# Kernel optimization log

Hardware: AMD Instinct MI355X
Metric: run time of the kernel (lower is better)

The kernel has to match this reference:

```python
import jax, jax.numpy as jnp
import numpy as np

D = 256      # d_model
K = 8        # knn neighbors
Q = 2048     # num queries
N = 32768    # num superpoints
H = 8        # mamba heads (d_inner/head_dim)
HD = 64      # head_dim
ST = 64      # state_size
DIN = H * HD                 # 512, expand*d_model
CONV = DIN + 2 * ST          # 640
NPROJ = 2 * DIN + 2 * ST + H # 1160
HID = 1024   # ffn hidden
NL = 2       # ssm layers
KC = 4       # conv kernel


def _ln(x, eps=1e-5):
    m = x.mean(-1, keepdims=True)
    v = ((x - m) ** 2).mean(-1, keepdims=True)
    return (x - m) * jax.lax.rsqrt(v + eps)


def _silu(x):
    return x * jax.nn.sigmoid(x)


def _mamba2(x, Win, Wconv, bconv, A_log, Dh, dtb, rmsw, Wout):
    # x: [B, L, D]; faithful HF Mamba2Mixer recurrent form
    B, L, _ = x.shape
    proj = x @ Win.T  # [B,L,NPROJ]
    z, xBC, dt = jnp.split(proj, [DIN, DIN + CONV], axis=-1)
    # causal depthwise conv1d, kernel KC, left pad KC-1
    xp = jnp.pad(xBC, ((0, 0), (KC - 1, 0), (0, 0)))
    conv = sum(xp[:, j:j + L, :] * Wconv[:, j] for j in range(KC))
    xBC = _silu(conv + bconv)
    xs, Bm, Cm = jnp.split(xBC, [DIN, DIN + ST], axis=-1)
    dt = jax.nn.softplus(dt + dtb)  # [B,L,H]
    A = -jnp.exp(A_log)             # [H]
    xh = xs.reshape(B, L, H, HD)
    dA = jnp.exp(dt * A)            # [B,L,H]
    dBx = dt[..., None, None] * Bm[:, :, None, None, :] * xh[..., None]  # [B,L,H,HD,ST]

    def step(h, inp):
        dA_t, dBx_t, C_t = inp
        h = h * dA_t[..., None, None] + dBx_t
        y = jnp.einsum('bhds,bs->bhd', h, C_t)
        return h, y

    h0 = jnp.zeros((B, H, HD, ST), x.dtype)
    _, ys = jax.lax.scan(step, h0, (dA.transpose(1, 0, 2),
                                    dBx.transpose(1, 0, 2, 3, 4),
                                    Cm.transpose(1, 0, 2)))
    y = ys.transpose(1, 0, 2, 3) + Dh[None, None, :, None] * xh
    y = y.reshape(B, L, DIN) * _silu(z)  # gated RMSNorm
    y = y * jax.lax.rsqrt((y * y).mean(-1, keepdims=True) + 1e-5) * rmsw
    return y @ Wout.T


def setup_inputs() -> dict:
    key = jax.random.key(0)
    ks = jax.random.split(key, 32)
    s = 0.02
    rn = lambda i, sh: jax.random.normal(ks[i], sh, jnp.float32) * s
    inp = {
        'query': jax.random.normal(ks[0], (Q, D), jnp.float32),
        'query_pos': jax.random.uniform(ks[1], (Q, 3), jnp.float32),
        'inst_feats': jax.random.normal(ks[2], (N, D), jnp.float32),
        'sp_coords': jax.random.uniform(ks[3], (N, 3), jnp.float32),
        'w_q': rn(4, (D, D)), 'w_v': rn(5, (D, D)), 'w_o': rn(6, (D, D)),
        'w_k': rn(7, (K, D)), 'w_b': jnp.zeros((K,), jnp.float32),
        'ssm_Win': rn(8, (NL, NPROJ, D)),
        'ssm_Wconv': rn(9, (NL, CONV, KC)),
        'ssm_bconv': jnp.zeros((NL, CONV), jnp.float32),
        'ssm_Alog': jnp.log(jnp.broadcast_to(jnp.arange(1, H + 1, dtype=jnp.float32), (NL, H))),
        'ssm_D': jnp.ones((NL, H), jnp.float32),
        'ssm_dtb': jax.random.uniform(ks[10], (NL, H), jnp.float32) * 0.1,
        'ssm_rmsw': jnp.ones((NL, DIN), jnp.float32),
        'ssm_Wout': rn(11, (NL, D, DIN)),
        'ffn_w1': rn(12, (HID, D)), 'ffn_b1': jnp.zeros((HID,), jnp.float32),
        'ffn_w2': rn(13, (D, HID)), 'ffn_b2': jnp.zeros((D,), jnp.float32),
        'order': jnp.stack([jax.random.permutation(ks[14], Q),
                            jax.random.permutation(ks[15], Q)]).astype(jnp.int32),
    }
    return inp


def reference(query, query_pos, inst_feats, sp_coords,
              w_q, w_v, w_o, w_k, w_b,
              ssm_Win, ssm_Wconv, ssm_bconv, ssm_Alog, ssm_D, ssm_dtb, ssm_rmsw, ssm_Wout,
              ffn_w1, ffn_b1, ffn_w2, ffn_b2, order):
    # --- MambaAggregation: KNN group + small-K softmax mixing ---
    d2 = (query_pos ** 2).sum(-1, keepdims=True) + (sp_coords ** 2).sum(-1)[None, :] \
         - 2.0 * query_pos @ sp_coords.T  # [Q,N]
    _, idx = jax.lax.top_k(-d2, K)        # [Q,K] nearest neighbors
    feat = inst_feats[idx]                # [Q,K,D]
    q = query @ w_q.T
    v = feat @ w_v.T
    kw = jax.nn.softmax(q @ w_k.T + w_b, axis=-1)          # [Q,K]
    w = jnp.einsum('qk,qd,qkd->qd', kw, q, v)
    x = _ln(w @ w_o.T + query)

    # --- SSM: serialize along 2 orders, Mamba2 mix, unsort, average ---
    inv = jnp.argsort(order, axis=1)  # [2,Q]
    for l in range(NL):
        sc = x
        xn = _ln(x)
        xs = xn[order]  # [2,Q,D], two serialization paths as batch
        y = _mamba2(xs, ssm_Win[l], ssm_Wconv[l], ssm_bconv[l], ssm_Alog[l],
                    ssm_D[l], ssm_dtb[l], ssm_rmsw[l], ssm_Wout[l])
        back = jnp.take_along_axis(y, inv[:, :, None], axis=1)  # undo sort
        x = _ln(sc + back.mean(0))

    # --- FFN ---
    h = jax.nn.gelu(x @ ffn_w1.T + ffn_b1, approximate=False) @ ffn_w2.T + ffn_b2
    return _ln(x + h)
```

## Files before the change

### kernel.cpp

```cpp
#include <hip/hip_runtime.h>
#include <cstdint>


typedef __attribute__((ext_vector_type(8))) short bf16x8;
typedef __attribute__((ext_vector_type(4))) float f32x4;
typedef unsigned short ushort_t;

__device__ __forceinline__ unsigned short f2bf(float f) {
  unsigned int u = __float_as_uint(f);
  u += 0x7fff + ((u >> 16) & 1);
  return (unsigned short)(u >> 16);
}
__device__ __forceinline__ float bf2f(unsigned short h) {
  return __uint_as_float(((unsigned int)h) << 16);
}

__global__ __launch_bounds__(256) void cvt_kernel(
    const float* __restrict__ src, unsigned short* __restrict__ hi,
    unsigned short* __restrict__ lo, int n4)
{
  const int i = blockIdx.x*256 + threadIdx.x;
  if (i < n4) {
    const float4 v = ((const float4*)src)[i];
    const unsigned short h0=f2bf(v.x), h1=f2bf(v.y), h2=f2bf(v.z), h3=f2bf(v.w);
    const unsigned short l0=f2bf(v.x-bf2f(h0)), l1=f2bf(v.y-bf2f(h1)),
                         l2=f2bf(v.z-bf2f(h2)), l3=f2bf(v.w-bf2f(h3));
    ((uint2*)hi)[i] = make_uint2((unsigned)h0 | ((unsigned)h1<<16),
                                 (unsigned)h2 | ((unsigned)h3<<16));
    ((uint2*)lo)[i] = make_uint2((unsigned)l0 | ((unsigned)l1<<16),
                                 (unsigned)l2 | ((unsigned)l3<<16));
  }
}

#define KNN_INS_U(ukv, uiv)                                                    \
  do {                                                                         \
    const unsigned int _k = (ukv); const int _v = (uiv);                       \
    const bool a0 = _k < k0;                                                   \
    const bool a1 = _k < k1;                                                   \
    const bool a2 = _k < k2;                                                   \
    const bool a3 = _k < k3;                                                   \
    const bool a4 = _k < k4;                                                   \
    const bool a5 = _k < k5;                                                   \
    const bool a6 = _k < k6;                                                   \
    k7 = a6 ? k6 : _k;              id7 = a6 ? id6 : _v;                       \
    k6 = a5 ? k5 : (a6 ? _k : k6);  id6 = a5 ? id5 : (a6 ? _v : id6);          \
    k5 = a4 ? k4 : (a5 ? _k : k5);  id5 = a4 ? id4 : (a5 ? _v : id5);          \
    k4 = a3 ? k3 : (a4 ? _k : k4);  id4 = a3 ? id3 : (a4 ? _v : id4);          \
    k3 = a2 ? k2 : (a3 ? _k : k3);  id3 = a2 ? id2 : (a3 ? _v : id3);          \
    k2 = a1 ? k1 : (a2 ? _k : k2);  id2 = a1 ? id1 : (a2 ? _v : id2);          \
    k1 = a0 ? k0 : (a1 ? _k : k1);  id1 = a0 ? id0 : (a1 ? _v : id1);          \
    k0 = a0 ? _k : k0;              id0 = a0 ? _v : id0;                       \
  } while (0)

__device__ __forceinline__ bool ulex_less(unsigned int k, int i,
                                          unsigned int kr, int ir) {
  return k < kr || (k == kr && i < ir);
}

#define KNN_INS_ULEX(ukv, uiv)                                                 \
  do {                                                                         \
    const unsigned int _k = (ukv); const int _v = (uiv);                       \
    const bool a0 = ulex_less(_k, _v, k0, id0);                                \
    const bool a1 = ulex_less(_k, _v, k1, id1);                                \
    const bool a2 = ulex_less(_k, _v, k2, id2);                                \
    const bool a3 = ulex_less(_k, _v, k3, id3);                                \
    const bool a4 = ulex_less(_k, _v, k4, id4);                                \
    const bool a5 = ulex_less(_k, _v, k5, id5);                                \
    const bool a6 = ulex_less(_k, _v, k6, id6);                                \
    k7 = a6 ? k6 : _k;              id7 = a6 ? id6 : _v;                       \
    k6 = a5 ? k5 : (a6 ? _k : k6);  id6 = a5 ? id5 : (a6 ? _v : id6);          \
    k5 = a4 ? k4 : (a5 ? _k : k5);  id5 = a4 ? id4 : (a5 ? _v : id5);          \
    k4 = a3 ? k3 : (a4 ? _k : k4);  id4 = a3 ? id3 : (a4 ? _v : id4);          \
    k3 = a2 ? k2 : (a3 ? _k : k3);  id3 = a2 ? id2 : (a3 ? _v : id3);          \
    k2 = a1 ? k1 : (a2 ? _k : k2);  id2 = a1 ? id1 : (a2 ? _v : id2);          \
    k1 = a0 ? k0 : (a1 ? _k : k1);  id1 = a0 ? id0 : (a1 ? _v : id1);          \
    k0 = a0 ? _k : k0;              id0 = a0 ? _v : id0;                       \
  } while (0)

#define KNN_RESET_U()                                                          \
  do {                                                                         \
    k0=k1=k2=k3=k4=k5=k6=k7 = 0xFFFFFFFFu;                                     \
    id0=id1=id2=id3=id4=id5=id6=id7 = 0x7fffffff;                              \
  } while (0)

__global__ void prep_kernel(const float* __restrict__ spos,
                            float4* __restrict__ P4)
{
#pragma clang fp contract(off)
  const int n = blockIdx.x*256 + threadIdx.x;
  if (n < 32768) {
    const float sx = spos[n*3+0], sy = spos[n*3+1], sz = spos[n*3+2];
    P4[n] = make_float4(sx, sy, sz, sx*sx + sy*sy + sz*sz);
  }
}

__global__ __launch_bounds__(256) void knn_kernel(
    const float* __restrict__ qpos, const float4* __restrict__ P4,
    int* __restrict__ idx_out)
{
#pragma clang fp contract(off)
  __shared__ unsigned int skey[32];
  __shared__ int          sidx[32];
  const int q = blockIdx.x, tid = threadIdx.x;
  const int wave = tid >> 6, lane = tid & 63;
  const float qx = qpos[q*3+0], qy = qpos[q*3+1], qz = qpos[q*3+2];
  const float qq = qx*qx + qy*qy + qz*qz;
  unsigned int k0,k1,k2,k3,k4,k5,k6,k7;
  int          id0,id1,id2,id3,id4,id5,id6,id7;
  KNN_RESET_U();
  const int base = wave << 13;
  for (int it = 0; it < 128; ++it) {
    const int nb = base + (it << 6);
    const float4 p = P4[nb + lane];
    const float dot = qx*p.x + qy*p.y + qz*p.z;
    const float d2 = (qq + p.w) - 2.0f*dot;
    unsigned int u = __float_as_uint(d2);
    u ^= (unsigned int)((int)u >> 31) | 0x80000000u;
    unsigned long long m = __ballot(u < k7);
    if (m) {
      do {
        const int l = __ffsll(m) - 1;
        m &= m - 1;
        const unsigned int uk = (unsigned int)__shfl((int)u, l);
        if (uk < k7) {
          KNN_INS_U(uk, nb + l);
        }
      } while (m);
    }
  }
  if (lane == 0) {
    skey[wave*8+0]=k0; skey[wave*8+1]=k1; skey[wave*8+2]=k2; skey[wave*8+3]=k3;
    skey[wave*8+4]=k4; skey[wave*8+5]=k5; skey[wave*8+6]=k6; skey[wave*8+7]=k7;
    sidx[wave*8+0]=id0; sidx[wave*8+1]=id1; sidx[wave*8+2]=id2; sidx[wave*8+3]=id3;
    sidx[wave*8+4]=id4; sidx[wave*8+5]=id5; sidx[wave*8+6]=id6; sidx[wave*8+7]=id7;
  }
  __syncthreads();
  if (tid == 0) {
    KNN_RESET_U();
    for (int s = 0; s < 32; ++s) {
      const unsigned int uk = skey[s];
      const int          ui = sidx[s];
      if (ulex_less(uk, ui, k7, id7)) KNN_INS_ULEX(uk, ui);
    }
    idx_out[q*8+0]=id0; idx_out[q*8+1]=id1; idx_out[q*8+2]=id2; idx_out[q*8+3]=id3;
    idx_out[q*8+4]=id4; idx_out[q*8+5]=id5; idx_out[q*8+6]=id6; idx_out[q*8+7]=id7;
  }
}

__global__ void inv_kernel(const int* __restrict__ order, int* __restrict__ inv)
{
  int i = blockIdx.x*blockDim.x + threadIdx.x;
  if (i < 4096) { int b = i >> 11, t = i & 2047; inv[(b<<11) + order[i]] = t; }
}

#define GBM 128
#define GBN 64
#define GBK 32
#define GLDK 40
__global__ __launch_bounds__(256) void gemm_mfma(
    const unsigned short* __restrict__ Ahp, const unsigned short* __restrict__ Alp,
    const int* __restrict__ rowmap,
    const unsigned short* __restrict__ Bhp, const unsigned short* __restrict__ Blp,
    const float* __restrict__ bias,
    float* __restrict__ Y, int M, int Nn, int Kd, int act)
{
  __shared__ unsigned short Ah[GBM*GLDK], Al[GBM*GLDK];
  __shared__ unsigned short Bh[GBN*GLDK], Bl[GBN*GLDK];
  const int tid = threadIdx.x;
  const int bm = blockIdx.x, bn = blockIdx.y;
  const int wid = tid >> 6, lane = tid & 63;
  const int wr = wid >> 1, wc = wid & 1;
  const int l15 = lane & 15, lk = (lane >> 4) << 3;

  const int sar = tid >> 1, sak = (tid & 1) << 4;
  const int agrow = bm*GBM + sar;
  const int asrc = rowmap ? rowmap[agrow] : agrow;
  const unsigned short* ArH = Ahp + (size_t)asrc * Kd + sak;
  const unsigned short* ArL = Alp + (size_t)asrc * Kd + sak;
  const int sbr = tid >> 2, sbk = (tid & 3) << 3;
  const int wrow = bn*GBN + sbr;
  const bool bok = (wrow < Nn);
  const unsigned short* BrH = Bhp + (size_t)(bok ? wrow : 0) * Kd + sbk;
  const unsigned short* BrL = Blp + (size_t)(bok ? wrow : 0) * Kd + sbk;

  f32x4 acc[4][2];
#pragma unroll
  for (int m = 0; m < 4; ++m)
#pragma unroll
    for (int n = 0; n < 2; ++n) acc[m][n] = (f32x4){0.f,0.f,0.f,0.f};

  const uint4 z4 = make_uint4(0u,0u,0u,0u);
  for (int k0 = 0; k0 < Kd; k0 += GBK) {
    const int ao = sar*GLDK + sak;
    *(uint4*)&Ah[ao]     = *(const uint4*)(ArH + k0);
    *(uint4*)&Ah[ao + 8] = *(const uint4*)(ArH + k0 + 8);
    *(uint4*)&Al[ao]     = *(const uint4*)(ArL + k0);
    *(uint4*)&Al[ao + 8] = *(const uint4*)(ArL + k0 + 8);
    const int bo = sbr*GLDK + sbk;
    *(uint4*)&Bh[bo] = bok ? *(const uint4*)(BrH + k0) : z4;
    *(uint4*)&Bl[bo] = bok ? *(const uint4*)(BrL + k0) : z4;
    __syncthreads();
    bf16x8 afh[4], afl[4], bfh[2], bfl[2];
#pragma unroll
    for (int m = 0; m < 4; ++m) {
      const int row = wr*64 + m*16 + l15;
      afh[m] = *(const bf16x8*)&Ah[row*GLDK + lk];
      afl[m] = *(const bf16x8*)&Al[row*GLDK + lk];
    }
#pragma unroll
    for (int n = 0; n < 2; ++n) {
      const int row = wc*32 + n*16 + l15;
      bfh[n] = *(const bf16x8*)&Bh[row*GLDK + lk];
      bfl[n] = *(const bf16x8*)&Bl[row*GLDK + lk];
    }
#pragma unroll
    for (int m = 0; m < 4; ++m)
#pragma unroll
      for (int n = 0; n < 2; ++n) {
        acc[m][n] = __builtin_amdgcn_mfma_f32_16x16x32_bf16(afh[m], bfh[n], acc[m][n], 0,0,0);
        acc[m][n] = __builtin_amdgcn_mfma_f32_16x16x32_bf16(afh[m], bfl[n], acc[m][n], 0,0,0);
        acc[m][n] = __builtin_amdgcn_mfma_f32_16x16x32_bf16(afl[m], bfh[n], acc[m][n], 0,0,0);
      }
    __syncthreads();
  }
  const int crow0 = bm*GBM + wr*64 + (lane >> 4)*4;
#pragma unroll
  for (int m = 0; m < 4; ++m) {
#pragma unroll
    for (int n = 0; n < 2; ++n) {
      const int col = bn*GBN + wc*32 + n*16 + l15;
      if (col < Nn) {
#pragma unroll
        for (int r = 0; r < 4; ++r) {
          float v = acc[m][n][r];
          if (bias) v += bias[col];
          if (act == 1) v = 0.5f*v*(1.f + erff(v*0.7071067811865475f));
          Y[(size_t)(crow0 + m*16 + r)*Nn + col] = v;
        }
      }
    }
  }
}

__global__ __launch_bounds__(256) void kwmix_kernel(
    const float* __restrict__ QP, const float* __restrict__ wk,
    const float* __restrict__ wb, const float* __restrict__ V,
    float* __restrict__ W)
{
  const int wave = threadIdx.x >> 6, lane = threadIdx.x & 63;
  const int q = blockIdx.x*4 + wave;
  float qv[4];
#pragma unroll
  for (int j = 0; j < 4; ++j) qv[j] = QP[(size_t)q*256 + lane + 64*j];
  float logit[8];
#pragma unroll
  for (int k = 0; k < 8; ++k) {
    float p = 0.f;
#pragma unroll
    for (int j = 0; j < 4; ++j) p += qv[j]*wk[k*256 + lane + 64*j];
    for (int off = 32; off; off >>= 1) p += __shfl_xor(p, off);
    logit[k] = p + wb[k];
  }
  float mx = logit[0];
#pragma unroll
  for (int k = 1; k < 8; ++k) mx = fmaxf(mx, logit[k]);
  float e[8]; float s = 0.f;
#pragma unroll
  for (int k = 0; k < 8; ++k) { e[k] = expf(logit[k]-mx); s += e[k]; }
  float inv = 1.f/s;
  float acc[4] = {0.f,0.f,0.f,0.f};
#pragma unroll
  for (int k = 0; k < 8; ++k) {
    float kwv = e[k]*inv;
#pragma unroll
    for (int j = 0; j < 4; ++j)
      acc[j] = fmaf(kwv, V[(size_t)(q*8+k)*256 + lane + 64*j], acc[j]);
  }
#pragma unroll
  for (int j = 0; j < 4; ++j)
    W[(size_t)q*256 + lane + 64*j] = qv[j]*acc[j];
}

__global__ __launch_bounds__(256) void ln_kernel(
    const float* __restrict__ a, const float* __restrict__ b,
    float* __restrict__ out, int rows)
{
  const int wave = threadIdx.x >> 6, lane = threadIdx.x & 63;
  const int row = blockIdx.x*4 + wave;
  if (row >= rows) return;
  float v[4];
#pragma unroll
  for (int j = 0; j < 4; ++j) {
    float x = a[(size_t)row*256 + lane + 64*j];
    if (b) x += b[(size_t)row*256 + lane + 64*j];
    v[j] = x;
  }
  float s = v[0]+v[1]+v[2]+v[3];
  for (int off = 32; off; off >>= 1) s += __shfl_xor(s, off);
  float m = s * (1.0f/256.0f);
  float t = 0.f;
#pragma unroll
  for (int j = 0; j < 4; ++j) { float d = v[j]-m; t += d*d; }
  for (int off = 32; off; off >>= 1) t += __shfl_xor(t, off);
  float r = rsqrtf(t * (1.0f/256.0f) + 1e-5f);
#pragma unroll
  for (int j = 0; j < 4; ++j)
    out[(size_t)row*256 + lane + 64*j] = (v[j]-m)*r;
}

__global__ __launch_bounds__(256) void ln_unsort_kernel(
    const float* __restrict__ OUTL, const int* __restrict__ INV,
    float* __restrict__ X)
{
  const int wave = threadIdx.x >> 6, lane = threadIdx.x & 63;
  const int q = blockIdx.x*4 + wave;
  const int i0 = INV[q], i1 = INV[2048 + q];
  float v[4];
#pragma unroll
  for (int j = 0; j < 4; ++j) {
    int d = lane + 64*j;
    v[j] = X[(size_t)q*256 + d]
         + 0.5f*(OUTL[(size_t)i0*256 + d] + OUTL[(size_t)(2048+i1)*256 + d]);
  }
  float s = v[0]+v[1]+v[2]+v[3];
  for (int off = 32; off; off >>= 1) s += __shfl_xor(s, off);
  float m = s * (1.0f/256.0f);
  float t = 0.f;
#pragma unroll
  for (int j = 0; j < 4; ++j) { float d = v[j]-m; t += d*d; }
  for (int off = 32; off; off >>= 1) t += __shfl_xor(t, off);
  float r = rsqrtf(t * (1.0f/256.0f) + 1e-5f);
#pragma unroll
  for (int j = 0; j < 4; ++j)
    X[(size_t)q*256 + lane + 64*j] = (v[j]-m)*r;
}

__global__ void conv_kernel(const float* __restrict__ PROJ,
    const float* __restrict__ Wc, const float* __restrict__ bc,
    float* __restrict__ XBC)
{
  const int c = threadIdx.x;
  const int bt = blockIdx.x;
  const int t = bt & 2047;
  float acc = bc[c];
#pragma unroll
  for (int j = 0; j < 4; ++j) {
    int d = j - 3;
    if (t + d >= 0)
      acc = fmaf(PROJ[(size_t)(bt + d)*1160 + 512 + c], Wc[c*4+j], acc);
  }
  XBC[(size_t)bt*640 + c] = acc / (1.f + expf(-acc));
}

__global__ void dta_kernel(const float* __restrict__ PROJ,
    const float* __restrict__ dtb, const float* __restrict__ Alog,
    float* __restrict__ Ddt, float* __restrict__ Dda)
{
  const int i = blockIdx.x*256 + threadIdx.x;
  const int bt = i >> 3, hh = i & 7;
  float x = PROJ[(size_t)bt*1160 + 1152 + hh] + dtb[hh];
  float dt = (x > 20.f) ? x : log1pf(expf(x));
  float A = -expf(Alog[hh]);
  Ddt[hh*4096 + bt] = dt;
  Dda[hh*4096 + bt] = expf(dt * A);
}

__global__ __launch_bounds__(64) void scan1_kernel(
    const float* __restrict__ XBC, const float* __restrict__ Ddt,
    const float* __restrict__ Dda, float* __restrict__ SCH, float* __restrict__ PC)
{
  const int blk = blockIdx.x;
  const int c = blk & 31, hh = (blk >> 5) & 7, b = blk >> 8;
  const int lane = threadIdx.x;
  const int t0 = (b << 11) + (c << 6);
  __shared__ float Bsh[64][64];
  __shared__ float Xsh[64][64];
  __shared__ float dAs[64], dts[64];
#pragma unroll
  for (int it = 0; it < 16; ++it) {
    int idx = it*64 + lane;
    int t = idx >> 4, c4 = (idx & 15) << 2;
    *(float4*)&Bsh[t][c4] = *(const float4*)&XBC[(size_t)(t0 + t)*640 + 512 + c4];
    *(float4*)&Xsh[t][c4] = *(const float4*)&XBC[(size_t)(t0 + t)*640 + (hh<<6) + c4];
  }
  dAs[lane] = Dda[hh*4096 + t0 + lane];
  dts[lane] = Ddt[hh*4096 + t0 + lane];
  __syncthreads();
  float h[64];
#pragma unroll
  for (int s = 0; s < 64; ++s) h[s] = 0.f;
  float p = 1.f;
  for (int t = 0; t < 64; ++t) {
    const float dA = dAs[t];
    const float u = dts[t]*Xsh[t][lane];
    p *= dA;
    const float4* B4 = (const float4*)&Bsh[t][0];
#pragma unroll
    for (int s4 = 0; s4 < 16; ++s4) {
      float4 bv = B4[s4];
      h[4*s4+0] = fmaf(h[4*s4+0], dA, bv.x*u);
      h[4*s4+1] = fmaf(h[4*s4+1], dA, bv.y*u);
      h[4*s4+2] = fmaf(h[4*s4+2], dA, bv.z*u);
      h[4*s4+3] = fmaf(h[4*s4+3], dA, bv.w*u);
    }
  }
  float* op = SCH + (size_t)blk*4096 + lane*64;
#pragma unroll
  for (int s4 = 0; s4 < 16; ++s4)
    ((float4*)op)[s4] = make_float4(h[4*s4], h[4*s4+1], h[4*s4+2], h[4*s4+3]);
  if (lane == 0) PC[blk] = p;
}

__global__ void combine_kernel(float* __restrict__ SCH, const float* __restrict__ PC)
{
  const int tid = blockIdx.x*256 + threadIdx.x;
  const int bh = tid >> 12, ds = tid & 4095;
  float h = 0.f;
  for (int cc = 0; cc < 32; ++cc) {
    size_t o = ((size_t)(bh*32 + cc) << 12) + ds;
    float s = SCH[o];
    SCH[o] = h;
    h = fmaf(h, PC[bh*32+cc], s);
  }
}

__global__ __launch_bounds__(64) void scan2_kernel(
    const float* __restrict__ XBC, const float* __restrict__ Ddt,
    const float* __restrict__ Dda, const float* __restrict__ HST,
    const float* __restrict__ Dm, float* __restrict__ Yout)
{
  const int blk = blockIdx.x;
  const int c = blk & 31, hh = (blk >> 5) & 7, b = blk >> 8;
  const int lane = threadIdx.x;
  const int t0 = (b << 11) + (c << 6);
  __shared__ float Bsh[64][64];
  __shared__ float Csh[64][64];
  __shared__ float Xsh[64][64];
  __shared__ float dAs[64], dts[64];
#pragma unroll
  for (int it = 0; it < 16; ++it) {
    int idx = it*64 + lane;
    int t = idx >> 4, c4 = (idx & 15) << 2;
    *(float4*)&Bsh[t][c4] = *(const float4*)&XBC[(size_t)(t0 + t)*640 + 512 + c4];
    *(float4*)&Csh[t][c4] = *(const float4*)&XBC[(size_t)(t0 + t)*640 + 576 + c4];
    *(float4*)&Xsh[t][c4] = *(const float4*)&XBC[(size_t)(t0 + t)*640 + (hh<<6) + c4];
  }
  dAs[lane] = Dda[hh*4096 + t0 + lane];
  dts[lane] = Ddt[hh*4096 + t0 + lane];
  const float Dh = Dm[hh];
  float h[64];
  const float4* hp = (const float4*)(HST + (size_t)blk*4096 + lane*64);
#pragma unroll
  for (int s4 = 0; s4 < 16; ++s4) {
    float4 t4 = hp[s4];
    h[4*s4+0]=t4.x; h[4*s4+1]=t4.y; h[4*s4+2]=t4.z; h[4*s4+3]=t4.w;
  }
  __syncthreads();
  for (int t = 0; t < 64; ++t) {
    const float dA = dAs[t];
    const float u = dts[t]*Xsh[t][lane];
    float y = 0.f;
    const float4* B4 = (const float4*)&Bsh[t][0];
    const float4* C4 = (const float4*)&Csh[t][0];
#pragma unroll
    for (int s4 = 0; s4 < 16; ++s4) {
      float4 bv = B4[s4];
      float4 cv = C4[s4];
      h[4*s4+0] = fmaf(h[4*s4+0], dA, bv.x*u); y = fmaf(cv.x, h[4*s4+0], y);
      h[4*s4+1] = fmaf(h[4*s4+1], dA, bv.y*u); y = fmaf(cv.y, h[4*s4+1], y);
      h[4*s4+2] = fmaf(h[4*s4+2], dA, bv.z*u); y = fmaf(cv.z, h[4*s4+2], y);
      h[4*s4+3] = fmaf(h[4*s4+3], dA, bv.w*u); y = fmaf(cv.w, h[4*s4+3], y);
    }
    Yout[(size_t)(t0 + t)*512 + (hh<<6) + lane] = y + Dh*Xsh[t][lane];
  }
}

__global__ __launch_bounds__(256) void gaterms_kernel(
    float* __restrict__ Y, const float* __restrict__ PROJ,
    const float* __restrict__ rmsw)
{
  const int wave = threadIdx.x >> 6, lane = threadIdx.x & 63;
  const int row = blockIdx.x*4 + wave;
  float v[8]; float ss = 0.f;
#pragma unroll
  for (int j = 0; j < 8; ++j) {
    float y = Y[(size_t)row*512 + lane + 64*j];
    float z = PROJ[(size_t)row*1160 + lane + 64*j];
    float g = y * (z / (1.f + expf(-z)));
    v[j] = g; ss += g*g;
  }
  for (int off = 32; off; off >>= 1) ss += __shfl_xor(ss, off);
  float r = rsqrtf(ss * (1.0f/512.0f) + 1e-5f);
#pragma unroll
  for (int j = 0; j < 8; ++j)
    Y[(size_t)row*512 + lane + 64*j] = v[j] * r * rmsw[lane + 64*j];
}

extern "C" void kernel_launch(void* const* d_in, const int* in_sizes, int n_in,
                              void* d_out, int out_size, void* d_ws, size_t ws_size,
                              hipStream_t stream)
{
  (void)in_sizes; (void)n_in; (void)out_size; (void)ws_size;
  const float* query = (const float*)d_in[0];
  const float* qpos  = (const float*)d_in[1];
  const float* feats = (const float*)d_in[2];
  const float* spos  = (const float*)d_in[3];
  const float* w_q   = (const float*)d_in[4];
  const float* w_v   = (const float*)d_in[5];
  const float* w_o   = (const float*)d_in[6];
  const float* w_k   = (const float*)d_in[7];
  const float* w_b   = (const float*)d_in[8];
  const float* Win   = (const float*)d_in[9];
  const float* Wconv = (const float*)d_in[10];
  const float* bconv = (const float*)d_in[11];
  const float* Alog  = (const float*)d_in[12];
  const float* Dm    = (const float*)d_in[13];
  const float* dtb   = (const float*)d_in[14];
  const float* rmsw  = (const float*)d_in[15];
  const float* Wout  = (const float*)d_in[16];
  const float* fw1   = (const float*)d_in[17];
  const float* fb1   = (const float*)d_in[18];
  const float* fw2   = (const float*)d_in[19];
  const float* fb2   = (const float*)d_in[20];
  const int*   order = (const int*)d_in[21];
  float* out = (float*)d_out;

  char* ws = (char*)d_ws;
  size_t off = 0;
  auto alloc = [&](size_t bytes) -> void* {
    void* p = ws + off;
    off = (off + bytes + 255) & ~(size_t)255;
    return p;
  };
  int*   IDX = (int*)alloc((size_t)2048*8*4);
  int*   INV = (int*)alloc((size_t)4096*4);
  float* PC  = (float*)alloc((size_t)512*4);
  float4* P4 = (float4*)alloc((size_t)32768*16);
  float* Ddt = (float*)alloc((size_t)4096*8*4);
  float* Dda = (float*)alloc((size_t)4096*8*4);
  float* QP  = (float*)alloc((size_t)2048*256*4);
  float* WB  = (float*)alloc((size_t)2048*256*4);
  float* WO  = (float*)alloc((size_t)2048*256*4);
  float* X   = (float*)alloc((size_t)2048*256*4);
  float* XN  = (float*)alloc((size_t)2048*256*4);
  float* U1  = (float*)alloc((size_t)4096*1160*4);
  float* U2  = (float*)alloc((size_t)4096*640*4);
  float* SCH = (float*)alloc((size_t)512*4096*4);
  float* Yb  = (float*)alloc((size_t)4096*512*4);
  float* U6  = (float*)alloc((size_t)4096*256*4);
  unsigned short* Qh  = (unsigned short*)alloc((size_t)2048*256*2);
  unsigned short* Ql  = (unsigned short*)alloc((size_t)2048*256*2);
  unsigned short* U7h = (unsigned short*)alloc((size_t)32768*256*2);
  unsigned short* U7l = (unsigned short*)alloc((size_t)32768*256*2);
  unsigned short* WBh = (unsigned short*)alloc((size_t)2048*256*2);
  unsigned short* WBl = (unsigned short*)alloc((size_t)2048*256*2);
  unsigned short* XNh = (unsigned short*)alloc((size_t)2048*256*2);
  unsigned short* XNl = (unsigned short*)alloc((size_t)2048*256*2);
  unsigned short* Ybh = (unsigned short*)alloc((size_t)4096*512*2);
  unsigned short* Ybl = (unsigned short*)alloc((size_t)4096*512*2);
  unsigned short* Xh  = (unsigned short*)alloc((size_t)2048*256*2);
  unsigned short* Xl  = (unsigned short*)alloc((size_t)2048*256*2);
  unsigned short* Wqh = (unsigned short*)alloc((size_t)256*256*2);
  unsigned short* Wql = (unsigned short*)alloc((size_t)256*256*2);
  unsigned short* Wvh = (unsigned short*)alloc((size_t)256*256*2);
  unsigned short* Wvl = (unsigned short*)alloc((size_t)256*256*2);
  unsigned short* Woh = (unsigned short*)alloc((size_t)256*256*2);
  unsigned short* Wol = (unsigned short*)alloc((size_t)256*256*2);
  unsigned short* Wih = (unsigned short*)alloc((size_t)2*1160*256*2);
  unsigned short* Wil = (unsigned short*)alloc((size_t)2*1160*256*2);
  unsigned short* Wuh = (unsigned short*)alloc((size_t)2*256*512*2);
  unsigned short* Wul = (unsigned short*)alloc((size_t)2*256*512*2);
  unsigned short* F1h = (unsigned short*)alloc((size_t)1024*256*2);
  unsigned short* F1l = (unsigned short*)alloc((size_t)1024*256*2);
  unsigned short* F2h = (unsigned short*)alloc((size_t)256*1024*2);
  unsigned short* F2l = (unsigned short*)alloc((size_t)256*1024*2);
  float* Vb   = U1;  float* PROJ = U1;
  float* XBC  = U2;  float* FFH  = U2;
  float* OUTL = U6;  float* FFO  = U6;
  unsigned short* FFHh = U7h;
  unsigned short* FFHl = U7l;

  auto cvt = [&](const float* s, unsigned short* h, unsigned short* l, int n) {
    cvt_kernel<<<(n/4 + 255)/256, 256, 0, stream>>>(s, h, l, n/4);
  };

  inv_kernel<<<16, 256, 0, stream>>>(order, INV);
  prep_kernel<<<128, 256, 0, stream>>>(spos, P4);
  knn_kernel<<<2048, 256, 0, stream>>>(qpos, P4, IDX);
  cvt(query, Qh, Ql, 2048*256);
  cvt(feats, U7h, U7l, 32768*256);
  cvt(w_q, Wqh, Wql, 256*256);
  cvt(w_v, Wvh, Wvl, 256*256);
  cvt(w_o, Woh, Wol, 256*256);
  cvt(Win, Wih, Wil, 2*1160*256);
  cvt(Wout, Wuh, Wul, 2*256*512);
  cvt(fw1, F1h, F1l, 1024*256);
  cvt(fw2, F2h, F2l, 256*1024);
  gemm_mfma<<<dim3(16,4), 256, 0, stream>>>(Qh, Ql, nullptr, Wqh, Wql, nullptr,
                                            QP, 2048,256,256,0);
  gemm_mfma<<<dim3(128,4), 256, 0, stream>>>(U7h, U7l, IDX, Wvh, Wvl, nullptr,
                                             Vb, 16384,256,256,0);
  kwmix_kernel<<<512, 256, 0, stream>>>(QP, w_k, w_b, Vb, WB);
  cvt(WB, WBh, WBl, 2048*256);
  gemm_mfma<<<dim3(16,4), 256, 0, stream>>>(WBh, WBl, nullptr, Woh, Wol, nullptr,
                                            WO, 2048,256,256,0);
  ln_kernel<<<512, 256, 0, stream>>>(WO, query, X, 2048);

  for (int l = 0; l < 2; ++l) {
    ln_kernel<<<512, 256, 0, stream>>>(X, nullptr, XN, 2048);
    cvt(XN, XNh, XNl, 2048*256);
    gemm_mfma<<<dim3(32,19), 256, 0, stream>>>(XNh, XNl, order,
                                               Wih + (size_t)l*1160*256,
                                               Wil + (size_t)l*1160*256,
                                               nullptr, PROJ, 4096,1160,256,0);
    conv_kernel<<<4096, 640, 0, stream>>>(PROJ, Wconv + l*640*4, bconv + l*640, XBC);
    dta_kernel<<<128, 256, 0, stream>>>(PROJ, dtb + l*8, Alog + l*8, Ddt, Dda);
    scan1_kernel<<<512, 64, 0, stream>>>(XBC, Ddt, Dda, SCH, PC);
    combine_kernel<<<256, 256, 0, stream>>>(SCH, PC);
    scan2_kernel<<<512, 64, 0, stream>>>(XBC, Ddt, Dda, SCH, Dm + l*8, Yb);
    gaterms_kernel<<<1024, 256, 0, stream>>>(Yb, PROJ, rmsw + l*512);
    cvt(Yb, Ybh, Ybl, 4096*512);
    gemm_mfma<<<dim3(32,4), 256, 0, stream>>>(Ybh, Ybl, nullptr,
                                              Wuh + (size_t)l*256*512,
                                              Wul + (size_t)l*256*512,
                                              nullptr, OUTL, 4096,256,512,0);
    ln_unsort_kernel<<<512, 256, 0, stream>>>(OUTL, INV, X);
  }

  cvt(X, Xh, Xl, 2048*256);
  gemm_mfma<<<dim3(16,16), 256, 0, stream>>>(Xh, Xl, nullptr, F1h, F1l, fb1,
                                             FFH, 2048,1024,256,1);
  cvt(FFH, FFHh, FFHl, 2048*1024);
  gemm_mfma<<<dim3(16,4), 256, 0, stream>>>(FFHh, FFHl, nullptr, F2h, F2l, fb2,
                                            FFO, 2048,256,1024,0);
  ln_kernel<<<512, 256, 0, stream>>>(FFO, X, out, 2048);
}
```

Measured before the change: 601.0 us.

## Fuse bf16 hi/lo splits into producer kernels and batch 4 queries per KNN block

Producer kernels (kwmix, ln, ln_unsort, gaterms, the FFN1 GEMM epilogue) now write the split bf16 hi/lo pair directly. This removes five separate cvt launches plus the fp32 intermediate round-trips. The KNN kernel now handles four queries per block with a prefetched P4 load, so each superpoint load is reused four times. The cost is higher register pressure from four top-8 lists and more divergent insertion loops per wave.

Result: no change. 607.4 us (+1.1%).

```diff
diff --git a/kernel.cpp b/kernel.cpp
--- a/kernel.cpp
+++ b/kernel.cpp
@@ -4,7 +4,6 @@
 
 typedef __attribute__((ext_vector_type(8))) short bf16x8;
 typedef __attribute__((ext_vector_type(4))) float f32x4;
-typedef unsigned short ushort_t;
 
 __device__ __forceinline__ unsigned short f2bf(float f) {
   unsigned int u = __float_as_uint(f);
@@ -32,24 +31,32 @@
   }
 }
 
-#define KNN_INS_U(ukv, uiv)                                                    \
+#define KNN_DECL(i)                                                            \
+  unsigned int k0_##i=0xFFFFFFFFu,k1_##i=0xFFFFFFFFu,k2_##i=0xFFFFFFFFu,       \
+               k3_##i=0xFFFFFFFFu,k4_##i=0xFFFFFFFFu,k5_##i=0xFFFFFFFFu,       \
+               k6_##i=0xFFFFFFFFu,k7_##i=0xFFFFFFFFu;                          \
+  int id0_##i=0x7fffffff,id1_##i=0x7fffffff,id2_##i=0x7fffffff,                \
+      id3_##i=0x7fffffff,id4_##i=0x7fffffff,id5_##i=0x7fffffff,                \
+      id6_##i=0x7fffffff,id7_##i=0x7fffffff
+
+#define KNN_INS_Q(i, ukv, uiv)                                                 \
   do {                                                                         \
     const unsigned int _k = (ukv); const int _v = (uiv);                       \
-    const bool a0 = _k < k0;                                                   \
-    const bool a1 = _k < k1;                                                   \
-    const bool a2 = _k < k2;                                                   \
-    const bool a3 = _k < k3;                                                   \
-    const bool a4 = _k < k4;                                                   \
-    const bool a5 = _k < k5;                                                   \
-    const bool a6 = _k < k6;                                                   \
-    k7 = a6 ? k6 : _k;              id7 = a6 ? id6 : _v;                       \
-    k6 = a5 ? k5 : (a6 ? _k : k6);  id6 = a5 ? id5 : (a6 ? _v : id6);          \
-    k5 = a4 ? k4 : (a5 ? _k : k5);  id5 = a4 ? id4 : (a5 ? _v : id5);          \
-    k4 = a3 ? k3 : (a4 ? _k : k4);  id4 = a3 ? id3 : (a4 ? _v : id4);          \
-    k3 = a2 ? k2 : (a3 ? _k : k3);  id3 = a2 ? id2 : (a3 ? _v : id3);          \
-    k2 = a1 ? k1 : (a2 ? _k : k2);  id2 = a1 ? id1 : (a2 ? _v : id2);          \
-    k1 = a0 ? k0 : (a1 ? _k : k1);  id1 = a0 ? id0 : (a1 ? _v : id1);          \
-    k0 = a0 ? _k : k0;              id0 = a0 ? _v : id0;                       \
+    const bool a0 = _k < k0_##i;                                               \
+    const bool a1 = _k < k1_##i;                                               \
+    const bool a2 = _k < k2_##i;                                               \
+    const bool a3 = _k < k3_##i;                                               \
+    const bool a4 = _k < k4_##i;                                               \
+    const bool a5 = _k < k5_##i;                                               \
+    const bool a6 = _k < k6_##i;                                               \
+    k7_##i = a6 ? k6_##i : _k;                  id7_##i = a6 ? id6_##i : _v;   \
+    k6_##i = a5 ? k5_##i : (a6 ? _k : k6_##i);  id6_##i = a5 ? id5_##i : (a6 ? _v : id6_##i); \
+    k5_##i = a4 ? k4_##i : (a5 ? _k : k5_##i);  id5_##i = a4 ? id4_##i : (a5 ? _v : id5_##i); \
+    k4_##i = a3 ? k3_##i : (a4 ? _k : k4_##i);  id4_##i = a3 ? id3_##i : (a4 ? _v : id4_##i); \
+    k3_##i = a2 ? k2_##i : (a3 ? _k : k3_##i);  id3_##i = a2 ? id2_##i : (a3 ? _v : id3_##i); \
+    k2_##i = a1 ? k1_##i : (a2 ? _k : k2_##i);  id2_##i = a1 ? id1_##i : (a2 ? _v : id2_##i); \
+    k1_##i = a0 ? k0_##i : (a1 ? _k : k1_##i);  id1_##i = a0 ? id0_##i : (a1 ? _v : id1_##i); \
+    k0_##i = a0 ? _k : k0_##i;                  id0_##i = a0 ? _v : id0_##i;   \
   } while (0)
 
 __device__ __forceinline__ bool ulex_less(unsigned int k, int i,
@@ -57,30 +64,48 @@
   return k < kr || (k == kr && i < ir);
 }
 
-#define KNN_INS_ULEX(ukv, uiv)                                                 \
+#define KNN_INS_LEXQ(i, ukv, uiv)                                              \
   do {                                                                         \
     const unsigned int _k = (ukv); const int _v = (uiv);                       \
-    const bool a0 = ulex_less(_k, _v, k0, id0);                                \
-    const bool a1 = ulex_less(_k, _v, k1, id1);                                \
-    const bool a2 = ulex_less(_k, _v, k2, id2);                                \
-    const bool a3 = ulex_less(_k, _v, k3, id3);                                \
-    const bool a4 = ulex_less(_k, _v, k4, id4);                                \
-    const bool a5 = ulex_less(_k, _v, k5, id5);                                \
-    const bool a6 = ulex_less(_k, _v, k6, id6);                                \
-    k7 = a6 ? k6 : _k;              id7 = a6 ? id6 : _v;                       \
-    k6 = a5 ? k5 : (a6 ? _k : k6);  id6 = a5 ? id5 : (a6 ? _v : id6);          \
-    k5 = a4 ? k4 : (a5 ? _k : k5);  id5 = a4 ? id4 : (a5 ? _v : id5);          \
-    k4 = a3 ? k3 : (a4 ? _k : k4);  id4 = a3 ? id3 : (a4 ? _v : id4);          \
-    k3 = a2 ? k2 : (a3 ? _k : k3);  id3 = a2 ? id2 : (a3 ? _v : id3);          \
-    k2 = a1 ? k1 : (a2 ? _k : k2);  id2 = a1 ? id1 : (a2 ? _v : id2);          \
-    k1 = a0 ? k0 : (a1 ? _k : k1);  id1 = a0 ? id0 : (a1 ? _v : id1);          \
-    k0 = a0 ? _k : k0;              id0 = a0 ? _v : id0;                       \
+    const bool a0 = ulex_less(_k, _v, k0_##i, id0_##i);                        \
+    const bool a1 = ulex_less(_k, _v, k1_##i, id1_##i);                        \
+    const bool a2 = ulex_less(_k, _v, k2_##i, id2_##i);                        \
+    const bool a3 = ulex_less(_k, _v, k3_##i, id3_##i);                        \
+    const bool a4 = ulex_less(_k, _v, k4_##i, id4_##i);                        \
+    const bool a5 = ulex_less(_k, _v, k5_##i, id5_##i);                        \
+    const bool a6 = ulex_less(_k, _v, k6_##i, id6_##i);                        \
+    k7_##i = a6 ? k6_##i : _k;                  id7_##i = a6 ? id6_##i : _v;   \
+    k6_##i = a5 ? k5_##i : (a6 ? _k : k6_##i);  id6_##i = a5 ? id5_##i : (a6 ? _v : id6_##i); \
+    k5_##i = a4 ? k4_##i : (a5 ? _k : k5_##i);  id5_##i = a4 ? id4_##i : (a5 ? _v : id5_##i); \
+    k4_##i = a3 ? k3_##i : (a4 ? _k : k4_##i);  id4_##i = a3 ? id3_##i : (a4 ? _v : id4_##i); \
+    k3_##i = a2 ? k2_##i : (a3 ? _k : k3_##i);  id3_##i = a2 ? id2_##i : (a3 ? _v : id3_##i); \
+    k2_##i = a1 ? k1_##i : (a2 ? _k : k2_##i);  id2_##i = a1 ? id1_##i : (a2 ? _v : id2_##i); \
+    k1_##i = a0 ? k0_##i : (a1 ? _k : k1_##i);  id1_##i = a0 ? id0_##i : (a1 ? _v : id1_##i); \
+    k0_##i = a0 ? _k : k0_##i;                  id0_##i = a0 ? _v : id0_##i;   \
   } while (0)
 
-#define KNN_RESET_U()                                                          \
+#define KNN_ROUND(i)                                                           \
   do {                                                                         \
-    k0=k1=k2=k3=k4=k5=k6=k7 = 0xFFFFFFFFu;                                     \
-    id0=id1=id2=id3=id4=id5=id6=id7 = 0x7fffffff;                              \
+    const float d2 = (qq##i + p.w)                                             \
+                   - 2.0f*(qx##i*p.x + qy##i*p.y + qz##i*p.z);                 \
+    unsigned int u = __float_as_uint(d2);                                      \
+    u ^= (unsigned int)((int)u >> 31) | 0x80000000u;                           \
+    unsigned long long m = __ballot(u < k7_##i);                               \
+    while (m) {                                                                \
+      const int l = __ffsll(m) - 1;                                            \
+      m &= m - 1;                                                              \
+      const unsigned int uk = (unsigned int)__shfl((int)u, l);                 \
+      if (uk < k7_##i) KNN_INS_Q(i, uk, nb + l);                               \
+    }                                                                          \
+  } while (0)
+
+#define KNN_STORE(i)                                                           \
+  do {                                                                         \
+    const int o = (i)*32 + wave*8;                                             \
+    skey[o+0]=k0_##i; skey[o+1]=k1_##i; skey[o+2]=k2_##i; skey[o+3]=k3_##i;    \
+    skey[o+4]=k4_##i; skey[o+5]=k5_##i; skey[o+6]=k6_##i; skey[o+7]=k7_##i;    \
+    sidx[o+0]=id0_##i; sidx[o+1]=id1_##i; sidx[o+2]=id2_##i; sidx[o+3]=id3_##i;\
+    sidx[o+4]=id4_##i; sidx[o+5]=id5_##i; sidx[o+6]=id6_##i; sidx[o+7]=id7_##i;\
   } while (0)
 
 __global__ void prep_kernel(const float* __restrict__ spos,
@@ -99,51 +124,41 @@
     int* __restrict__ idx_out)
 {
 #pragma clang fp contract(off)
-  __shared__ unsigned int skey[32];
-  __shared__ int          sidx[32];
-  const int q = blockIdx.x, tid = threadIdx.x;
+  __shared__ unsigned int skey[128];
+  __shared__ int          sidx[128];
+  const int q0 = blockIdx.x << 2, tid = threadIdx.x;
   const int wave = tid >> 6, lane = tid & 63;
-  const float qx = qpos[q*3+0], qy = qpos[q*3+1], qz = qpos[q*3+2];
-  const float qq = qx*qx + qy*qy + qz*qz;
-  unsigned int k0,k1,k2,k3,k4,k5,k6,k7;
-  int          id0,id1,id2,id3,id4,id5,id6,id7;
-  KNN_RESET_U();
+  const float qx0 = qpos[(q0+0)*3+0], qy0 = qpos[(q0+0)*3+1], qz0 = qpos[(q0+0)*3+2];
+  const float qx1 = qpos[(q0+1)*3+0], qy1 = qpos[(q0+1)*3+1], qz1 = qpos[(q0+1)*3+2];
+  const float qx2 = qpos[(q0+2)*3+0], qy2 = qpos[(q0+2)*3+1], qz2 = qpos[(q0+2)*3+2];
+  const float qx3 = qpos[(q0+3)*3+0], qy3 = qpos[(q0+3)*3+1], qz3 = qpos[(q0+3)*3+2];
+  const float qq0 = qx0*qx0 + qy0*qy0 + qz0*qz0;
+  const float qq1 = qx1*qx1 + qy1*qy1 + qz1*qz1;
+  const float qq2 = qx2*qx2 + qy2*qy2 + qz2*qz2;
+  const float qq3 = qx3*qx3 + qy3*qy3 + qz3*qz3;
+  KNN_DECL(0); KNN_DECL(1); KNN_DECL(2); KNN_DECL(3);
   const int base = wave << 13;
+  float4 p = P4[base + lane];
+  float4 pn = p;
   for (int it = 0; it < 128; ++it) {
+    if (it < 127) pn = P4[base + ((it+1) << 6) + lane];
     const int nb = base + (it << 6);
-    const float4 p = P4[nb + lane];
-    const float dot = qx*p.x + qy*p.y + qz*p.z;
-    const float d2 = (qq + p.w) - 2.0f*dot;
-    unsigned int u = __float_as_uint(d2);
-    u ^= (unsigned int)((int)u >> 31) | 0x80000000u;
-    unsigned long long m = __ballot(u < k7);
-    if (m) {
-      do {
-        const int l = __ffsll(m) - 1;
-        m &= m - 1;
-        const unsigned int uk = (unsigned int)__shfl((int)u, l);
-        if (uk < k7) {
-          KNN_INS_U(uk, nb + l);
-        }
-      } while (m);
+    KNN_ROUND(0); KNN_ROUND(1); KNN_ROUND(2); KNN_ROUND(3);
+    p = pn;
+  }
+  if (lane == 0) { KNN_STORE(0); KNN_STORE(1); KNN_STORE(2); KNN_STORE(3); }
+  __syncthreads();
+  if (tid < 4) {
+    KNN_DECL(m);
+    const int o = tid*32;
+    for (int s = 0; s < 32; ++s) {
+      const unsigned int uk = skey[o + s];
+      const int          ui = sidx[o + s];
+      if (ulex_less(uk, ui, k7_m, id7_m)) KNN_INS_LEXQ(m, uk, ui);
     }
-  }
-  if (lane == 0) {
-    skey[wave*8+0]=k0; skey[wave*8+1]=k1; skey[wave*8+2]=k2; skey[wave*8+3]=k3;
-    skey[wave*8+4]=k4; skey[wave*8+5]=k5; skey[wave*8+6]=k6; skey[wave*8+7]=k7;
-    sidx[wave*8+0]=id0; sidx[wave*8+1]=id1; sidx[wave*8+2]=id2; sidx[wave*8+3]=id3;
-    sidx[wave*8+4]=id4; sidx[wave*8+5]=id5; sidx[wave*8+6]=id6; sidx[wave*8+7]=id7;
-  }
-  __syncthreads();
-  if (tid == 0) {
-    KNN_RESET_U();
-    for (int s = 0; s < 32; ++s) {
-      const unsigned int uk = skey[s];
-      const int          ui = sidx[s];
-      if (ulex_less(uk, ui, k7, id7)) KNN_INS_ULEX(uk, ui);
-    }
-    idx_out[q*8+0]=id0; idx_out[q*8+1]=id1; idx_out[q*8+2]=id2; idx_out[q*8+3]=id3;
-    idx_out[q*8+4]=id4; idx_out[q*8+5]=id5; idx_out[q*8+6]=id6; idx_out[q*8+7]=id7;
+    const int ob = (q0 + tid)*8;
+    idx_out[ob+0]=id0_m; idx_out[ob+1]=id1_m; idx_out[ob+2]=id2_m; idx_out[ob+3]=id3_m;
+    idx_out[ob+4]=id4_m; idx_out[ob+5]=id5_m; idx_out[ob+6]=id6_m; idx_out[ob+7]=id7_m;
   }
 }
 
@@ -162,7 +177,9 @@
     const int* __restrict__ rowmap,
     const unsigned short* __restrict__ Bhp, const unsigned short* __restrict__ Blp,
     const float* __restrict__ bias,
-    float* __restrict__ Y, int M, int Nn, int Kd, int act)
+    float* __restrict__ Y,
+    unsigned short* __restrict__ Yh, unsigned short* __restrict__ Yl,
+    int M, int Nn, int Kd, int act)
 {
   __shared__ unsigned short Ah[GBM*GLDK], Al[GBM*GLDK];
   __shared__ unsigned short Bh[GBN*GLDK], Bl[GBN*GLDK];
@@ -235,7 +252,13 @@
           float v = acc[m][n][r];
           if (bias) v += bias[col];
           if (act == 1) v = 0.5f*v*(1.f + erff(v*0.7071067811865475f));
-          Y[(size_t)(crow0 + m*16 + r)*Nn + col] = v;
+          const size_t idx = (size_t)(crow0 + m*16 + r)*Nn + col;
+          if (Yh) {
+            const unsigned short h = f2bf(v);
+            Yh[idx] = h; Yl[idx] = f2bf(v - bf2f(h));
+          } else {
+            Y[idx] = v;
+          }
         }
       }
     }
@@ -245,7 +268,7 @@
 __global__ __launch_bounds__(256) void kwmix_kernel(
     const float* __restrict__ QP, const float* __restrict__ wk,
     const float* __restrict__ wb, const float* __restrict__ V,
-    float* __restrict__ W)
+    unsigned short* __restrict__ Wh, unsigned short* __restrict__ Wl)
 {
   const int wave = threadIdx.x >> 6, lane = threadIdx.x & 63;
   const int q = blockIdx.x*4 + wave;
@@ -277,13 +300,19 @@
       acc[j] = fmaf(kwv, V[(size_t)(q*8+k)*256 + lane + 64*j], acc[j]);
   }
 #pragma unroll
-  for (int j = 0; j < 4; ++j)
-    W[(size_t)q*256 + lane + 64*j] = qv[j]*acc[j];
+  for (int j = 0; j < 4; ++j) {
+    const float v = qv[j]*acc[j];
+    const unsigned short h = f2bf(v);
+    const size_t o = (size_t)q*256 + lane + 64*j;
+    Wh[o] = h; Wl[o] = f2bf(v - bf2f(h));
+  }
 }
 
 __global__ __launch_bounds__(256) void ln_kernel(
     const float* __restrict__ a, const float* __restrict__ b,
-    float* __restrict__ out, int rows)
+    float* __restrict__ out,
+    unsigned short* __restrict__ oh, unsigned short* __restrict__ ol,
+    int rows)
 {
   const int wave = threadIdx.x >> 6, lane = threadIdx.x & 63;
   const int row = blockIdx.x*4 + wave;
@@ -304,13 +333,18 @@
   for (int off = 32; off; off >>= 1) t += __shfl_xor(t, off);
   float r = rsqrtf(t * (1.0f/256.0f) + 1e-5f);
 #pragma unroll
-  for (int j = 0; j < 4; ++j)
-    out[(size_t)row*256 + lane + 64*j] = (v[j]-m)*r;
+  for (int j = 0; j < 4; ++j) {
+    const float y = (v[j]-m)*r;
+    const size_t o = (size_t)row*256 + lane + 64*j;
+    if (out) out[o] = y;
+    if (oh) { const unsigned short h = f2bf(y); oh[o] = h; ol[o] = f2bf(y - bf2f(h)); }
+  }
 }
 
 __global__ __launch_bounds__(256) void ln_unsort_kernel(
     const float* __restrict__ OUTL, const int* __restrict__ INV,
-    float* __restrict__ X)
+    float* __restrict__ X,
+    unsigned short* __restrict__ oh, unsigned short* __restrict__ ol)
 {
   const int wave = threadIdx.x >> 6, lane = threadIdx.x & 63;
   const int q = blockIdx.x*4 + wave;
@@ -331,8 +365,12 @@
   for (int off = 32; off; off >>= 1) t += __shfl_xor(t, off);
   float r = rsqrtf(t * (1.0f/256.0f) + 1e-5f);
 #pragma unroll
-  for (int j = 0; j < 4; ++j)
-    X[(size_t)q*256 + lane + 64*j] = (v[j]-m)*r;
+  for (int j = 0; j < 4; ++j) {
+    const float y = (v[j]-m)*r;
+    const size_t o = (size_t)q*256 + lane + 64*j;
+    X[o] = y;
+    if (oh) { const unsigned short h = f2bf(y); oh[o] = h; ol[o] = f2bf(y - bf2f(h)); }
+  }
 }
 
 __global__ void conv_kernel(const float* __restrict__ PROJ,
@@ -476,8 +514,9 @@
 }
 
 __global__ __launch_bounds__(256) void gaterms_kernel(
-    float* __restrict__ Y, const float* __restrict__ PROJ,
-    const float* __restrict__ rmsw)
+    const float* __restrict__ Y, const float* __restrict__ PROJ,
+    const float* __restrict__ rmsw,
+    unsigned short* __restrict__ Oh, unsigned short* __restrict__ Ol)
 {
   const int wave = threadIdx.x >> 6, lane = threadIdx.x & 63;
   const int row = blockIdx.x*4 + wave;
@@ -492,8 +531,12 @@
   for (int off = 32; off; off >>= 1) ss += __shfl_xor(ss, off);
   float r = rsqrtf(ss * (1.0f/512.0f) + 1e-5f);
 #pragma unroll
-  for (int j = 0; j < 8; ++j)
-    Y[(size_t)row*512 + lane + 64*j] = v[j] * r * rmsw[lane + 64*j];
+  for (int j = 0; j < 8; ++j) {
+    const float o = v[j] * r * rmsw[lane + 64*j];
+    const unsigned short h = f2bf(o);
+    const size_t ix = (size_t)row*512 + lane + 64*j;
+    Oh[ix] = h; Ol[ix] = f2bf(o - bf2f(h));
+  }
 }
 
 extern "C" void kernel_launch(void* const* d_in, const int* in_sizes, int n_in,
@@ -539,10 +582,8 @@
   float* Ddt = (float*)alloc((size_t)4096*8*4);
   float* Dda = (float*)alloc((size_t)4096*8*4);
   float* QP  = (float*)alloc((size_t)2048*256*4);
-  float* WB  = (float*)alloc((size_t)2048*256*4);
   float* WO  = (float*)alloc((size_t)2048*256*4);
   float* X   = (float*)alloc((size_t)2048*256*4);
-  float* XN  = (float*)alloc((size_t)2048*256*4);
   float* U1  = (float*)alloc((size_t)4096*1160*4);
   float* U2  = (float*)alloc((size_t)4096*640*4);
   float* SCH = (float*)alloc((size_t)512*4096*4);
@@ -575,7 +616,7 @@
   unsigned short* F2h = (unsigned short*)alloc((size_t)256*1024*2);
   unsigned short* F2l = (unsigned short*)alloc((size_t)256*1024*2);
   float* Vb   = U1;  float* PROJ = U1;
-  float* XBC  = U2;  float* FFH  = U2;
+  float* XBC  = U2;
   float* OUTL = U6;  float* FFO  = U6;
   unsigned short* FFHh = U7h;
   unsigned short* FFHl = U7l;
@@ -586,7 +627,7 @@
 
   inv_kernel<<<16, 256, 0, stream>>>(order, INV);
   prep_kernel<<<128, 256, 0, stream>>>(spos, P4);
-  knn_kernel<<<2048, 256, 0, stream>>>(qpos, P4, IDX);
+  knn_kernel<<<512, 256, 0, stream>>>(qpos, P4, IDX);
   cvt(query, Qh, Ql, 2048*256);
   cvt(feats, U7h, U7l, 32768*256);
   cvt(w_q, Wqh, Wql, 256*256);
@@ -597,41 +638,40 @@
   cvt(fw1, F1h, F1l, 1024*256);
   cvt(fw2, F2h, F2l, 256*1024);
   gemm_mfma<<<dim3(16,4), 256, 0, stream>>>(Qh, Ql, nullptr, Wqh, Wql, nullptr,
-                                            QP, 2048,256,256,0);
+                                            QP, nullptr, nullptr, 2048,256,256,0);
   gemm_mfma<<<dim3(128,4), 256, 0, stream>>>(U7h, U7l, IDX, Wvh, Wvl, nullptr,
-                                             Vb, 16384,256,256,0);
-  kwmix_kernel<<<512, 256, 0, stream>>>(QP, w_k, w_b, Vb, WB);
-  cvt(WB, WBh, WBl, 2048*256);
+                                             Vb, nullptr, nullptr, 16384,256,256,0);
+  kwmix_kernel<<<512, 256, 0, stream>>>(QP, w_k, w_b, Vb, WBh, WBl);
   gemm_mfma<<<dim3(16,4), 256, 0, stream>>>(WBh, WBl, nullptr, Woh, Wol, nullptr,
-                                            WO, 2048,256,256,0);
-  ln_kernel<<<512, 256, 0, stream>>>(WO, query, X, 2048);
+                                            WO, nullptr, nullptr, 2048,256,256,0);
+  ln_kernel<<<512, 256, 0, stream>>>(WO, query, X, nullptr, nullptr, 2048);
 
   for (int l = 0; l < 2; ++l) {
-    ln_kernel<<<512, 256, 0, stream>>>(X, nullptr, XN, 2048);
-    cvt(XN, XNh, XNl, 2048*256);
+    ln_kernel<<<512, 256, 0, stream>>>(X, nullptr, nullptr, XNh, XNl, 2048);
     gemm_mfma<<<dim3(32,19), 256, 0, stream>>>(XNh, XNl, order,
                                                Wih + (size_t)l*1160*256,
                                                Wil + (size_t)l*1160*256,
-                                               nullptr, PROJ, 4096,1160,256,0);
+                                               nullptr, PROJ, nullptr, nullptr,
+                                               4096,1160,256,0);
     conv_kernel<<<4096, 640, 0, stream>>>(PROJ, Wconv + l*640*4, bconv + l*640, XBC);
     dta_kernel<<<128, 256, 0, stream>>>(PROJ, dtb + l*8, Alog + l*8, Ddt, Dda);
     scan1_kernel<<<512, 64, 0, stream>>>(XBC, Ddt, Dda, SCH, PC);
     combine_kernel<<<256, 256, 0, stream>>>(SCH, PC);
     scan2_kernel<<<512, 64, 0, stream>>>(XBC, Ddt, Dda, SCH, Dm + l*8, Yb);
-    gaterms_kernel<<<1024, 256, 0, stream>>>(Yb, PROJ, rmsw + l*512);
-    cvt(Yb, Ybh, Ybl, 4096*512);
+    gaterms_kernel<<<1024, 256, 0, stream>>>(Yb, PROJ, rmsw + l*512, Ybh, Ybl);
     gemm_mfma<<<dim3(32,4), 256, 0, stream>>>(Ybh, Ybl, nullptr,
                                               Wuh + (size_t)l*256*512,
                                               Wul + (size_t)l*256*512,
-                                              nullptr, OUTL, 4096,256,512,0);
-    ln_unsort_kernel<<<512, 256, 0, stream>>>(OUTL, INV, X);
-  }
-
-  cvt(X, Xh, Xl, 2048*256);
+                                              nullptr, OUTL, nullptr, nullptr,
+                                              4096,256,512,0);
+    ln_unsort_kernel<<<512, 256, 0, stream>>>(OUTL, INV, X,
+                                              (l==1) ? Xh : nullptr,
+                                              (l==1) ? Xl : nullptr);
+  }
+
   gemm_mfma<<<dim3(16,16), 256, 0, stream>>>(Xh, Xl, nullptr, F1h, F1l, fb1,
-                                             FFH, 2048,1024,256,1);
-  cvt(FFH, FFHh, FFHl, 2048*1024);
+                                             nullptr, FFHh, FFHl, 2048,1024,256,1);
   gemm_mfma<<<dim3(16,4), 256, 0, stream>>>(FFHh, FFHl, nullptr, F2h, F2l, fb2,
-                                            FFO, 2048,256,1024,0);
-  ln_kernel<<<512, 256, 0, stream>>>(FFO, X, out, 2048);
-}
+                                            FFO, nullptr, nullptr, 2048,256,1024,0);
+  ln_kernel<<<512, 256, 0, stream>>>(FFO, X, out, nullptr, nullptr, 2048);
+}
```
